# Optimization experiments

Hardware: AMD Instinct MI355X
Metric: run time of the kernel (lower is better)

Reference implementation:

```python
import jax, jax.numpy as jnp
import numpy as np

EPS = 1e-12  # matches torch F.normalize default eps
TEMP = 0.1


def _gram(x):
    # L2-normalize rows; for unit vectors 1 - 0.5*||xi-xj||^2 == xi . xj
    n = x / jnp.maximum(jnp.linalg.norm(x, axis=-1, keepdims=True), EPS)
    return n @ n.T  # [N, N]


def setup_inputs() -> dict:
    key = jax.random.key(0)
    k1, k2, k3, k4 = jax.random.split(key, 4)
    N, D = 4096, 512
    return {
        "fm_rgb": jax.random.normal(k1, (N, D), dtype=jnp.float32),
        "fm_depth": jax.random.normal(k2, (N, D), dtype=jnp.float32),
        "fm_ir": jax.random.normal(k3, (N, D), dtype=jnp.float32),
        "fm_t": jax.random.normal(k4, (N, D), dtype=jnp.float32),
    }


def reference(fm_rgb, fm_depth, fm_ir, fm_t):
    G_rgb = _gram(fm_rgb)
    G_depth = _gram(fm_depth)
    G_ir = _gram(fm_ir)
    G_t = _gram(fm_t)
    inv_t = 1.0 / TEMP
    loss_rgb = jnp.mean((G_t * inv_t - G_rgb * inv_t) ** 2)
    loss_depth = jnp.mean((G_t * inv_t - G_depth * inv_t) ** 2)
    loss_ir = jnp.mean((G_t * inv_t - G_ir * inv_t) ** 2)
    return loss_rgb + loss_depth + loss_ir
```

## Files before the change

### kernel.cpp

```cpp
#include <hip/hip_runtime.h>
#include <hip/hip_bf16.h>


typedef __attribute__((ext_vector_type(4))) float floatx4;
typedef __attribute__((ext_vector_type(2))) long long llx2;
typedef __attribute__((ext_vector_type(8))) int intx8;

#define N_ROWS 4096
#define DDIM   512
#define LOSS_SCALE 9.094947017729282e-11f

__device__ __forceinline__ const float* sel_mod(int mod, const float* a,
                                                const float* b, const float* c,
                                                const float* d) {
  return mod == 0 ? a : mod == 1 ? b : mod == 2 ? c : d;
}

__device__ __forceinline__ float bfr(float x) {
  __hip_bfloat16 h = __float2bfloat16(x);
  unsigned short u = *(unsigned short*)&h;
  return __uint_as_float(((unsigned int)u) << 16);
}

__global__ __launch_bounds__(512) void preprocess_kernel(
    const float* __restrict__ in0, const float* __restrict__ in1,
    const float* __restrict__ in2, const float* __restrict__ in3,
    unsigned char* __restrict__ nT8, float* __restrict__ out) {
  int mod = blockIdx.y;
  int k0 = blockIdx.x * 64;
  const float* X = sel_mod(mod, in0, in1, in2, in3) + (size_t)k0 * DDIM;

  if (blockIdx.x == 0 && blockIdx.y == 0 && threadIdx.x == 0)
    out[0] = 0.f;

  __shared__ float rsc[64];
  __shared__ unsigned int t8[512 * 17];

  int t = threadIdx.x;
  int a = t >> 5;
  int bg = t & 31;

  float4 v[4][4];
#pragma unroll
  for (int q = 0; q < 4; ++q)
#pragma unroll
    for (int p = 0; p < 4; ++p)
      v[q][p] = ((const float4*)(X + (size_t)(4 * a + q) * DDIM + p * 128))[bg];

  float ss[4];
#pragma unroll
  for (int q = 0; q < 4; ++q) {
    float acc = 0.f;
#pragma unroll
    for (int p = 0; p < 4; ++p) {
      float4 u = v[q][p];
      acc += u.x * u.x + u.y * u.y + u.z * u.z + u.w * u.w;
    }
    ss[q] = acc;
  }
#pragma unroll
  for (int off = 16; off > 0; off >>= 1)
#pragma unroll
    for (int q = 0; q < 4; ++q) ss[q] += __shfl_down(ss[q], off, 32);
  if (bg == 0) {
#pragma unroll
    for (int q = 0; q < 4; ++q)
      rsc[4 * a + q] = 16.0f / fmaxf(sqrtf(ss[q]), 1e-12f);
  }
  __syncthreads();

  float sc[4];
#pragma unroll
  for (int q = 0; q < 4; ++q) sc[q] = rsc[4 * a + q];

#pragma unroll
  for (int p = 0; p < 4; ++p)
#pragma unroll
    for (int j = 0; j < 4; ++j) {
      float f0 = bfr(((const float*)&v[0][p])[j] * sc[0]);
      float f1 = bfr(((const float*)&v[1][p])[j] * sc[1]);
      float f2 = bfr(((const float*)&v[2][p])[j] * sc[2]);
      float f3 = bfr(((const float*)&v[3][p])[j] * sc[3]);
      unsigned int pk = __builtin_amdgcn_cvt_pk_fp8_f32(f0, f1, 0, 0);
      pk = __builtin_amdgcn_cvt_pk_fp8_f32(f2, f3, pk, 1);
      t8[(p * 128 + bg * 4 + j) * 17 + a] = pk;
    }
  __syncthreads();

  size_t rbase = (size_t)(mod * 64 + blockIdx.x) * 32768;
#pragma unroll
  for (int it = 0; it < 4; ++it) {
    int idx = it * 512 + t;
    int col = idx >> 2;
    int g = idx & 3;
    uint4 o;
    o.x = t8[col * 17 + g * 4 + 0];
    o.y = t8[col * 17 + g * 4 + 1];
    o.z = t8[col * 17 + g * 4 + 2];
    o.w = t8[col * 17 + g * 4 + 3];
    *(uint4*)(nT8 + rbase + (size_t)idx * 16) = o;
  }
}

__device__ __forceinline__ intx8 ldfrag(const unsigned char* __restrict__ p) {
  intx8 r;
  *(llx2*)&r = *(const llx2*)p;
  *((llx2*)&r + 1) = *(const llx2*)(p + 16);
  return r;
}

__global__ __launch_bounds__(64) void gram_frob_kernel(
    const unsigned char* __restrict__ nT8, float* __restrict__ out) {
  int bx = blockIdx.x;
  int u = (bx & 7) * 168 + (bx >> 3);
  int job = u >> 2;
  int quad = u & 3;
  int mh = quad >> 1;
  int nh = quad & 1;

  int rem = job, ti = 7, tj = 7;
  for (int i = 0; i < 8; ++i) {
    int rowlen = 7 + 10 * (7 - i);
    if (rem < rowlen) {
      if (rem < 7) {
        ti = i; tj = i;
      } else {
        int r2 = rem - 7;
        ti = i; tj = i + 1 + r2 / 10;
        rem = r2 % 10;
      }
      break;
    }
    rem -= rowlen;
  }

  int pa_, pb_, a0, b0;
  float wgt;
  if (ti == tj) {
    if (rem < 4) { pa_ = pb_ = rem; wgt = (rem == 3) ? 3.f : 1.f; }
    else         { pa_ = 3; pb_ = rem - 4; wgt = -2.f; }
    a0 = ti * 64; b0 = ti * 64;
  } else {
    if (rem < 4) {
      pa_ = pb_ = rem; wgt = (rem == 3) ? 6.f : 2.f;
      a0 = ti * 64; b0 = tj * 64;
    } else {
      int k = rem - 4;
      pa_ = 3; pb_ = k >> 1; wgt = -2.f;
      if (k & 1) { a0 = tj * 64; b0 = ti * 64; }
      else       { a0 = ti * 64; b0 = tj * 64; }
    }
  }

  int lane = threadIdx.x;
  int lm = lane & 15;
  int lq = lane >> 4;

  size_t lkb = ((size_t)(lq >> 1) * 512 + lm) * 64 + (size_t)(lq & 1) * 32;
  const unsigned char* pA0 =
      nT8 + (size_t)pa_ * 2097152 + lkb + (size_t)(a0 + 32 * mh) * 64;
  const unsigned char* pA1 = pA0 + 16 * 64;
  const unsigned char* pB0 =
      nT8 + (size_t)pb_ * 2097152 + lkb + (size_t)(b0 + 32 * nh) * 64;
  const unsigned char* pB1 = pB0 + 16 * 64;
#define CHUNK_STRIDE 65536

  floatx4 zero = {0.f, 0.f, 0.f, 0.f};
  floatx4 acc[2][2];
  acc[0][0] = zero; acc[0][1] = zero; acc[1][0] = zero; acc[1][1] = zero;

#define MFMA4(AR, BR)                                                        \
  do {                                                                       \
    __builtin_amdgcn_s_setprio(1);                                           \
    acc[0][0] = __builtin_amdgcn_mfma_scale_f32_16x16x128_f8f6f4(            \
        AR[0], BR[0], acc[0][0], 0, 0, 0, 0x7F, 0, 0x7F);                    \
    acc[0][1] = __builtin_amdgcn_mfma_scale_f32_16x16x128_f8f6f4(            \
        AR[0], BR[1], acc[0][1], 0, 0, 0, 0x7F, 0, 0x7F);                    \
    acc[1][0] = __builtin_amdgcn_mfma_scale_f32_16x16x128_f8f6f4(            \
        AR[1], BR[0], acc[1][0], 0, 0, 0, 0x7F, 0, 0x7F);                    \
    acc[1][1] = __builtin_amdgcn_mfma_scale_f32_16x16x128_f8f6f4(            \
        AR[1], BR[1], acc[1][1], 0, 0, 0, 0x7F, 0, 0x7F);                    \
    __builtin_amdgcn_s_setprio(0);                                           \
  } while (0)

  intx8 ae[2], be[2], ao[2], bo[2];
  ae[0] = ldfrag(pA0); ae[1] = ldfrag(pA1);
  be[0] = ldfrag(pB0); be[1] = ldfrag(pB1);
  for (int ch = 0; ch < 30; ch += 2) {
    pA0 += CHUNK_STRIDE; pA1 += CHUNK_STRIDE;
    pB0 += CHUNK_STRIDE; pB1 += CHUNK_STRIDE;
    ao[0] = ldfrag(pA0); ao[1] = ldfrag(pA1);
    bo[0] = ldfrag(pB0); bo[1] = ldfrag(pB1);
    MFMA4(ae, be);
    pA0 += CHUNK_STRIDE; pA1 += CHUNK_STRIDE;
    pB0 += CHUNK_STRIDE; pB1 += CHUNK_STRIDE;
    ae[0] = ldfrag(pA0); ae[1] = ldfrag(pA1);
    be[0] = ldfrag(pB0); be[1] = ldfrag(pB1);
    MFMA4(ao, bo);
  }
  pA0 += CHUNK_STRIDE; pA1 += CHUNK_STRIDE;
  pB0 += CHUNK_STRIDE; pB1 += CHUNK_STRIDE;
  ao[0] = ldfrag(pA0); ao[1] = ldfrag(pA1);
  bo[0] = ldfrag(pB0); bo[1] = ldfrag(pB1);
  MFMA4(ae, be);
  MFMA4(ao, bo);

  float s = 0.f;
#pragma unroll
  for (int mi = 0; mi < 2; ++mi)
#pragma unroll
    for (int ni = 0; ni < 2; ++ni)
#pragma unroll
      for (int r = 0; r < 4; ++r) {
        float v = acc[mi][ni][r];
        s += v * v;
      }
#pragma unroll
  for (int off = 32; off > 0; off >>= 1) s += __shfl_down(s, off, 64);
  if (lane == 0)
    atomicAdd(out, wgt * LOSS_SCALE * s);
}

extern "C" void kernel_launch(void* const* d_in, const int* in_sizes, int n_in,
                              void* d_out, int out_size, void* d_ws, size_t ws_size,
                              hipStream_t stream) {
  const float* in_rgb   = (const float*)d_in[0];
  const float* in_depth = (const float*)d_in[1];
  const float* in_ir    = (const float*)d_in[2];
  const float* in_t     = (const float*)d_in[3];

  unsigned char* nT8 = (unsigned char*)d_ws;

  preprocess_kernel<<<dim3(64, 4), 512, 0, stream>>>(
      in_rgb, in_depth, in_ir, in_t, nT8, (float*)d_out);
  gram_frob_kernel<<<dim3(1344), 64, 0, stream>>>(nT8, (float*)d_out);
}
```

Before: 117.7 us.

## Split K across four waves per 64x64 tile with LDS partial-sum reduction

Each block now handles a full 64x64 tile job with 256 threads. Each of the four waves processes a quarter of the K dimension, holding a 4x4 set of MFMA accumulators, instead of one 64-thread block per 32x32 quadrant working over all of K. Partial accumulators are summed through 64KB of shared memory before squaring, and one atomic is issued per block. This is meant to reuse A/B fragments across a wider output tile and cut the serial K chain per wave. In exchange it adds LDS traffic and barriers, raises register pressure, and launches only 336 blocks.

```diff
diff --git a/kernel.cpp b/kernel.cpp
--- a/kernel.cpp
+++ b/kernel.cpp
@@ -109,14 +109,13 @@
   return r;
 }
 
-__global__ __launch_bounds__(64) void gram_frob_kernel(
+__global__ __launch_bounds__(256) void gram_frob_kernel(
     const unsigned char* __restrict__ nT8, float* __restrict__ out) {
+  __shared__ float pacc[4][4096];
+  __shared__ float red[4];
+
   int bx = blockIdx.x;
-  int u = (bx & 7) * 168 + (bx >> 3);
-  int job = u >> 2;
-  int quad = u & 3;
-  int mh = quad >> 1;
-  int nh = quad & 1;
+  int job = (bx & 7) * 42 + (bx >> 3);
 
   int rem = job, ti = 7, tj = 7;
   for (int i = 0; i < 8; ++i) {
@@ -152,73 +151,89 @@
     }
   }
 
-  int lane = threadIdx.x;
+  int t = threadIdx.x;
+  int w = t >> 6;
+  int lane = t & 63;
   int lm = lane & 15;
   int lq = lane >> 4;
 
-  size_t lkb = ((size_t)(lq >> 1) * 512 + lm) * 64 + (size_t)(lq & 1) * 32;
-  const unsigned char* pA0 =
-      nT8 + (size_t)pa_ * 2097152 + lkb + (size_t)(a0 + 32 * mh) * 64;
-  const unsigned char* pA1 = pA0 + 16 * 64;
-  const unsigned char* pB0 =
-      nT8 + (size_t)pb_ * 2097152 + lkb + (size_t)(b0 + 32 * nh) * 64;
-  const unsigned char* pB1 = pB0 + 16 * 64;
+  size_t lkb =
+      ((size_t)(w * 16 + (lq >> 1)) * 512 + lm) * 64 + (size_t)(lq & 1) * 32;
+  const unsigned char* pA =
+      nT8 + (size_t)pa_ * 2097152 + lkb + (size_t)a0 * 64;
+  const unsigned char* pB =
+      nT8 + (size_t)pb_ * 2097152 + lkb + (size_t)b0 * 64;
+#define FRAG_STRIDE 1024
 #define CHUNK_STRIDE 65536
+#define ADV do { pA += CHUNK_STRIDE; pB += CHUNK_STRIDE; } while (0)
 
   floatx4 zero = {0.f, 0.f, 0.f, 0.f};
-  floatx4 acc[2][2];
-  acc[0][0] = zero; acc[0][1] = zero; acc[1][0] = zero; acc[1][1] = zero;
-
-#define MFMA4(AR, BR)                                                        \
-  do {                                                                       \
-    __builtin_amdgcn_s_setprio(1);                                           \
-    acc[0][0] = __builtin_amdgcn_mfma_scale_f32_16x16x128_f8f6f4(            \
-        AR[0], BR[0], acc[0][0], 0, 0, 0, 0x7F, 0, 0x7F);                    \
-    acc[0][1] = __builtin_amdgcn_mfma_scale_f32_16x16x128_f8f6f4(            \
-        AR[0], BR[1], acc[0][1], 0, 0, 0, 0x7F, 0, 0x7F);                    \
-    acc[1][0] = __builtin_amdgcn_mfma_scale_f32_16x16x128_f8f6f4(            \
-        AR[1], BR[0], acc[1][0], 0, 0, 0, 0x7F, 0, 0x7F);                    \
-    acc[1][1] = __builtin_amdgcn_mfma_scale_f32_16x16x128_f8f6f4(            \
-        AR[1], BR[1], acc[1][1], 0, 0, 0, 0x7F, 0, 0x7F);                    \
-    __builtin_amdgcn_s_setprio(0);                                           \
+  floatx4 acc[4][4];
+#pragma unroll
+  for (int mi = 0; mi < 4; ++mi)
+#pragma unroll
+    for (int ni = 0; ni < 4; ++ni) acc[mi][ni] = zero;
+
+  intx8 ae[4], be[4], ao[4], bo[4];
+
+#define LDALL(AR, BR)                                                       \
+  do {                                                                      \
+    _Pragma("unroll")                                                       \
+    for (int f_ = 0; f_ < 4; ++f_) {                                        \
+      AR[f_] = ldfrag(pA + f_ * FRAG_STRIDE);                               \
+      BR[f_] = ldfrag(pB + f_ * FRAG_STRIDE);                               \
+    }                                                                       \
   } while (0)
 
-  intx8 ae[2], be[2], ao[2], bo[2];
-  ae[0] = ldfrag(pA0); ae[1] = ldfrag(pA1);
-  be[0] = ldfrag(pB0); be[1] = ldfrag(pB1);
-  for (int ch = 0; ch < 30; ch += 2) {
-    pA0 += CHUNK_STRIDE; pA1 += CHUNK_STRIDE;
-    pB0 += CHUNK_STRIDE; pB1 += CHUNK_STRIDE;
-    ao[0] = ldfrag(pA0); ao[1] = ldfrag(pA1);
-    bo[0] = ldfrag(pB0); bo[1] = ldfrag(pB1);
-    MFMA4(ae, be);
-    pA0 += CHUNK_STRIDE; pA1 += CHUNK_STRIDE;
-    pB0 += CHUNK_STRIDE; pB1 += CHUNK_STRIDE;
-    ae[0] = ldfrag(pA0); ae[1] = ldfrag(pA1);
-    be[0] = ldfrag(pB0); be[1] = ldfrag(pB1);
-    MFMA4(ao, bo);
-  }
-  pA0 += CHUNK_STRIDE; pA1 += CHUNK_STRIDE;
-  pB0 += CHUNK_STRIDE; pB1 += CHUNK_STRIDE;
-  ao[0] = ldfrag(pA0); ao[1] = ldfrag(pA1);
-  bo[0] = ldfrag(pB0); bo[1] = ldfrag(pB1);
-  MFMA4(ae, be);
-  MFMA4(ao, bo);
+#define MFMA16(AR, BR)                                                      \
+  do {                                                                      \
+    __builtin_amdgcn_s_setprio(1);                                          \
+    _Pragma("unroll")                                                       \
+    for (int mi_ = 0; mi_ < 4; ++mi_)                                       \
+      _Pragma("unroll")                                                     \
+      for (int ni_ = 0; ni_ < 4; ++ni_)                                     \
+        acc[mi_][ni_] = __builtin_amdgcn_mfma_scale_f32_16x16x128_f8f6f4(   \
+            AR[mi_], BR[ni_], acc[mi_][ni_], 0, 0, 0, 0x7F, 0, 0x7F);       \
+    __builtin_amdgcn_s_setprio(0);                                          \
+  } while (0)
+
+  LDALL(ae, be);
+#pragma unroll
+  for (int ch = 0; ch < 6; ch += 2) {
+    ADV;
+    LDALL(ao, bo);
+    MFMA16(ae, be);
+    ADV;
+    LDALL(ae, be);
+    MFMA16(ao, bo);
+  }
+  ADV;
+  LDALL(ao, bo);
+  MFMA16(ae, be);
+  MFMA16(ao, bo);
+
+#pragma unroll
+  for (int mi = 0; mi < 4; ++mi)
+#pragma unroll
+    for (int ni = 0; ni < 4; ++ni)
+#pragma unroll
+      for (int r = 0; r < 4; ++r)
+        pacc[w][r * 1024 + (mi * 4 + ni) * 64 + lane] = acc[mi][ni][r];
+  __syncthreads();
 
   float s = 0.f;
 #pragma unroll
-  for (int mi = 0; mi < 2; ++mi)
-#pragma unroll
-    for (int ni = 0; ni < 2; ++ni)
-#pragma unroll
-      for (int r = 0; r < 4; ++r) {
-        float v = acc[mi][ni][r];
-        s += v * v;
-      }
+  for (int it = 0; it < 16; ++it) {
+    int idx = it * 256 + t;
+    float v = pacc[0][idx] + pacc[1][idx] + pacc[2][idx] + pacc[3][idx];
+    s += v * v;
+  }
 #pragma unroll
   for (int off = 32; off > 0; off >>= 1) s += __shfl_down(s, off, 64);
-  if (lane == 0)
-    atomicAdd(out, wgt * LOSS_SCALE * s);
+  if (lane == 0) red[w] = s;
+  __syncthreads();
+  if (t == 0)
+    atomicAdd(out, wgt * LOSS_SCALE * (red[0] + red[1] + red[2] + red[3]));
 }
 
 extern "C" void kernel_launch(void* const* d_in, const int* in_sizes, int n_in,
@@ -233,5 +248,5 @@
 
   preprocess_kernel<<<dim3(64, 4), 512, 0, stream>>>(
       in_rgb, in_depth, in_ir, in_t, nT8, (float*)d_out);
-  gram_frob_kernel<<<dim3(1344), 64, 0, stream>>>(nT8, (float*)d_out);
-}
+  gram_frob_kernel<<<dim3(336), 256, 0, stream>>>(nT8, (float*)d_out);
+}
```

Result: faster. 97.56 us, median of 2 (-17.1%).
